# Optimization experiments

Hardware: AMD Instinct MI355X
Metric: run time of the kernel (lower is better)

The kernel has to match this reference:

```python
import jax, jax.numpy as jnp
import numpy as np

NUM_QUANTIZERS = 8
CODEBOOK_SIZE = 1024
DIM = 64
B, N = 8, 8192


def setup_inputs() -> dict:
    key = jax.random.key(0)
    kx, kc = jax.random.split(key)
    x = jax.random.normal(kx, (B, N, DIM), dtype=jnp.float32)
    # one codebook per quantizer stage (shared_codebook=False)
    codebooks = jax.random.normal(kc, (NUM_QUANTIZERS, CODEBOOK_SIZE, DIM), dtype=jnp.float32)
    return {"x": x, "codebooks": codebooks}


def reference(x, codebooks):
    """Residual VQ: sequential nearest-codebook lookup with residual subtraction.

    x:         [b, n, d]
    codebooks: [Q, K, d]
    returns quantized_out: [b, n, d]
    """

    def step(carry, cb):
        residual, qout = carry                       # [b,n,d], [b,n,d]
        # squared euclidean distances, [b,n,K]
        r_sq = jnp.sum(residual * residual, axis=-1, keepdims=True)
        c_sq = jnp.sum(cb * cb, axis=-1)             # [K]
        dots = jnp.einsum('bnd,kd->bnk', residual, cb)
        dist = r_sq - 2.0 * dots + c_sq              # [b,n,K]
        idx = jnp.argmin(dist, axis=-1)              # [b,n]
        quant = cb[idx]                              # [b,n,d] gather
        # straight-through estimator (VectorQuantize forward)
        quant_st = residual + jax.lax.stop_gradient(quant - residual)
        new_residual = residual - jax.lax.stop_gradient(quant)
        return (new_residual, qout + quant_st), idx

    init = (x, jnp.zeros_like(x))
    (residual, quantized_out), all_indices = jax.lax.scan(step, init, codebooks)
    return quantized_out
```

## Files before the change

kernel.cpp:

```cpp
#include <hip/hip_runtime.h>

#define NQ 8
#define KCODES 1024
#define D 64
#define CHUNK 64
#define TPB 256
#define TOKPB 64
#define BIAS 96.0f

using short8 = __attribute__((ext_vector_type(8))) short;
using f32x4  = __attribute__((ext_vector_type(4))) float;

static __device__ __forceinline__ unsigned bf16_rne_bits(float f) {
    unsigned u = __float_as_uint(f);
    return (u + 0x7fffu + ((u >> 16) & 1u)) >> 16;
}
static __device__ __forceinline__ unsigned umn(unsigned a, unsigned b) { return a < b ? a : b; }
static __device__ __forceinline__ unsigned umx(unsigned a, unsigned b) { return a > b ? a : b; }
static __device__ __forceinline__ unsigned umed3(unsigned a, unsigned b, unsigned c) {
    unsigned d;
    asm("v_med3_u32 %0, %1, %2, %3" : "=v"(d) : "v"(a), "v"(b), "v"(c));
    return d;
}

__global__ __launch_bounds__(256) void prep_cb(const float* __restrict__ cb,
                                               int4* __restrict__ ws_cb) {
    int id = blockIdx.x * 256 + threadIdx.x;
    int n_rel = id & 63;
    int plane = (id >> 6) & 15;
    int ch    = (id >> 10) & 15;
    int q     = id >> 14;
    int g = plane & 3, kt = (plane >> 2) & 1, term = plane >> 3;
    int n = ch * CHUNK + n_rel;
    const float* src = cb + ((size_t)(q * KCODES + n)) * D + kt * 32 + g * 8;
    union { short s[8]; int4 v; } u;
    #pragma unroll
    for (int j = 0; j < 8; ++j) {
        float f = -src[j];
        unsigned hb = bf16_rne_bits(f);
        if (term == 0) {
            u.s[j] = (short)hb;
        } else {
            float lo = f - __uint_as_float(hb << 16);
            u.s[j] = (short)bf16_rne_bits(lo);
        }
    }
    ws_cb[id] = u.v;
}

__global__ __launch_bounds__(256) void prep_csq(const float* __restrict__ cb,
                                                float* __restrict__ ws_csq,
                                                float* __restrict__ ws_csqh) {
    int id = blockIdx.x * 256 + threadIdx.x;
    const float* c = cb + (size_t)id * D;
    float s0 = 0.f, s1 = 0.f, s2 = 0.f, s3 = 0.f;
    #pragma unroll
    for (int j = 0; j < 16; ++j) {
        s0 = fmaf(c[4*j+0], c[4*j+0], s0);
        s1 = fmaf(c[4*j+1], c[4*j+1], s1);
        s2 = fmaf(c[4*j+2], c[4*j+2], s2);
        s3 = fmaf(c[4*j+3], c[4*j+3], s3);
    }
    float cs = (s0 + s1) + (s2 + s3);
    ws_csq[id]  = cs;
    ws_csqh[id] = 0.5f * cs + BIAS;
}

__global__ __launch_bounds__(TPB, 4) void rvq_mfma(
    const float* __restrict__ x,
    const float* __restrict__ cb,
    const int4* __restrict__ ws_cb,
    const float* __restrict__ ws_csq,
    float* __restrict__ out)
{
    __shared__ __align__(16) float lds_resid[TOKPB * 68];
    __shared__ __align__(16) float lds_csqh_q[KCODES];
    __shared__ unsigned lds_cand[2][TOKPB * 3];
    __shared__ int      lds_pick[TOKPB];

    const int tid   = threadIdx.x;
    const int lane  = tid & 63;
    const int wave  = tid >> 6;
    const int group = wave >> 1;
    const int half  = wave & 1;
    const int g     = lane >> 4;
    const int c     = lane & 15;
    const int tok0  = blockIdx.x * TOKPB;
    const float* ws_csqh = ws_csq + 8192;

    {
        const int t = tid >> 2, part = tid & 3;
        const float4* xp = (const float4*)(x + (size_t)(tok0 + t) * D + part * 16);
        float4* rr = (float4*)(lds_resid + t * 68 + part * 16);
        #pragma unroll
        for (int k2 = 0; k2 < 4; ++k2) rr[k2] = xp[k2];
    }

    const int lid = (g << 6) + (half << 4) + c;
    const int sdo = (half << 4) + c;

    for (int q = 0; q < NQ; ++q) {
        {
            const float4 v = *(const float4*)(ws_csqh + (q << 10) + (tid << 2));
            *(float4*)(lds_csqh_q + (tid << 2)) = v;
        }
        __syncthreads();

        short8 ah0[2], ah1[2], al0[2], al1[2];
        #pragma unroll
        for (int s = 0; s < 2; ++s) {
            const float* rr = lds_resid + (group * 32 + s * 16 + c) * 68;
            float4 f0 = *(const float4*)(rr + 8 * g);
            float4 f1 = *(const float4*)(rr + 8 * g + 4);
            float4 f2 = *(const float4*)(rr + 32 + 8 * g);
            float4 f3 = *(const float4*)(rr + 36 + 8 * g);
            const float* v0 = (const float*)&f0;
            const float* v1 = (const float*)&f1;
            const float* v2 = (const float*)&f2;
            const float* v3 = (const float*)&f3;
            #pragma unroll
            for (int j = 0; j < 4; ++j) {
                float a = v0[j], b = v1[j], e = v2[j], f = v3[j];
                unsigned ha = bf16_rne_bits(a);
                unsigned hb = bf16_rne_bits(b);
                unsigned he = bf16_rne_bits(e);
                unsigned hf = bf16_rne_bits(f);
                ah0[s][j]   = (short)ha;  ah0[s][4+j] = (short)hb;
                ah1[s][j]   = (short)he;  ah1[s][4+j] = (short)hf;
                al0[s][j]   = (short)bf16_rne_bits(a - __uint_as_float(ha << 16));
                al0[s][4+j] = (short)bf16_rne_bits(b - __uint_as_float(hb << 16));
                al1[s][j]   = (short)bf16_rne_bits(e - __uint_as_float(he << 16));
                al1[s][4+j] = (short)bf16_rne_bits(f - __uint_as_float(hf << 16));
            }
        }

        unsigned T1[2][4], T2[2][4], T3[2][4];
        #pragma unroll
        for (int s = 0; s < 2; ++s)
            #pragma unroll
            for (int r = 0; r < 4; ++r) { T1[s][r] = 0xFFFFFFFFu; T2[s][r] = 0xFFFFFFFFu; T3[s][r] = 0xFFFFFFFFu; }

        const int4* fpq = ws_cb + ((size_t)q << 14) + lid;
        short8 nb0 = *(const short8*)(fpq);
        short8 nb1 = *(const short8*)(fpq + 256);
        short8 nb2 = *(const short8*)(fpq + 512);
        short8 nb3 = *(const short8*)(fpq + 768);
        #pragma unroll 1
        for (int ch = 0; ch < 32; ++ch) {
            const short8 bh0 = nb0, bh1 = nb1, bl0 = nb2, bl1 = nb3;
            if (ch < 31) {
                const int chn = ch + 1;
                const int4* fpn = fpq + ((chn >> 1) << 10) + ((chn & 1) << 5);
                nb0 = *(const short8*)(fpn);
                nb1 = *(const short8*)(fpn + 256);
                nb2 = *(const short8*)(fpn + 512);
                nb3 = *(const short8*)(fpn + 768);
            }
            const int cv = (ch << 5) + sdo;
            const float sd = lds_csqh_q[cv];
            const unsigned codev = (unsigned)cv;
            #pragma unroll
            for (int s = 0; s < 2; ++s) {
                f32x4 acc = {sd, sd, sd, sd};
                acc = __builtin_amdgcn_mfma_f32_16x16x32_bf16(ah0[s], bh0, acc, 0, 0, 0);
                acc = __builtin_amdgcn_mfma_f32_16x16x32_bf16(ah1[s], bh1, acc, 0, 0, 0);
                acc = __builtin_amdgcn_mfma_f32_16x16x32_bf16(al0[s], bh0, acc, 0, 0, 0);
                acc = __builtin_amdgcn_mfma_f32_16x16x32_bf16(ah0[s], bl0, acc, 0, 0, 0);
                acc = __builtin_amdgcn_mfma_f32_16x16x32_bf16(al1[s], bh1, acc, 0, 0, 0);
                acc = __builtin_amdgcn_mfma_f32_16x16x32_bf16(ah1[s], bl1, acc, 0, 0, 0);
                #pragma unroll
                for (int r = 0; r < 4; ++r) {
                    const unsigned p = (__float_as_uint(acc[r]) & 0xFFFFFC00u) | codev;
                    const unsigned t1o = T1[s][r], t2o = T2[s][r];
                    T1[s][r] = umn(t1o, p);
                    T2[s][r] = umed3(t1o, t2o, p);
                    T3[s][r] = umed3(t2o, T3[s][r], p);
                }
            }
        }

        #pragma unroll
        for (int st = 1; st <= 8; st <<= 1) {
            #pragma unroll
            for (int s = 0; s < 2; ++s) {
                #pragma unroll
                for (int r = 0; r < 4; ++r) {
                    unsigned o1 = (unsigned)__shfl_xor((int)T1[s][r], st);
                    unsigned o2 = (unsigned)__shfl_xor((int)T2[s][r], st);
                    unsigned o3 = (unsigned)__shfl_xor((int)T3[s][r], st);
                    unsigned x1 = umn(T1[s][r], o1), y1 = umx(T1[s][r], o1);
                    unsigned x2 = umn(T2[s][r], o2), y2 = umx(T2[s][r], o2);
                    unsigned x3 = umn(T3[s][r], o3);
                    T1[s][r] = x1;
                    T3[s][r] = umed3(y1, x2, umn(y2, x3));
                    T2[s][r] = umn(y1, x2);
                }
            }
        }

        if (c == 0) {
            #pragma unroll
            for (int s = 0; s < 2; ++s)
                #pragma unroll
                for (int r = 0; r < 4; ++r) {
                    const int idx = (group * 32 + s * 16 + g * 4 + r) * 3;
                    lds_cand[half][idx + 0] = T1[s][r];
                    lds_cand[half][idx + 1] = T2[s][r];
                    lds_cand[half][idx + 2] = T3[s][r];
                }
        }
        __syncthreads();

        {
            const int t4  = lane >> 2;
            const int sel = lane & 3;
            const int row = group * 32 + half * 16 + t4;
            unsigned a1 = lds_cand[0][row * 3 + 0];
            unsigned a2 = lds_cand[0][row * 3 + 1];
            unsigned a3 = lds_cand[0][row * 3 + 2];
            unsigned b1 = lds_cand[1][row * 3 + 0];
            unsigned b2 = lds_cand[1][row * 3 + 1];
            unsigned b3 = lds_cand[1][row * 3 + 2];
            unsigned x1 = umn(a1, b1), y1 = umx(a1, b1);
            unsigned x2 = umn(a2, b2), y2 = umx(a2, b2);
            unsigned x3 = umn(a3, b3);
            unsigned m1 = x1;
            unsigned m2 = umn(y1, x2);
            unsigned m3 = umed3(y1, x2, umn(y2, x3));
            const unsigned psel = (sel == 0) ? m1 : ((sel == 1) ? m2 : m3);
            const int cd = (int)(psel & 1023u);

            const float4* rrv = (const float4*)(lds_resid + row * 68);
            const float4* cpv = (const float4*)(cb + ((size_t)(q * KCODES + cd)) * D);
            float ax = 0.f, ay = 0.f, az = 0.f, aw = 0.f;
            #pragma unroll
            for (int j = 0; j < 16; ++j) {
                float4 rv = rrv[j];
                float4 cv = cpv[j];
                ax = fmaf(rv.x, cv.x, ax);
                ay = fmaf(rv.y, cv.y, ay);
                az = fmaf(rv.z, cv.z, az);
                aw = fmaf(rv.w, cv.w, aw);
            }
            float dot = (ax + ay) + (az + aw);
            float dd = fmaf(dot, -2.0f, ws_csq[q * KCODES + cd]);

            const int base = lane & ~3;
            float d0 = __shfl(dd, base);
            float d1 = __shfl(dd, base + 1);
            float d2 = __shfl(dd, base + 2);
            int cc0 = (int)(m1 & 1023u);
            int cc1 = (int)(m2 & 1023u);
            int cc2 = (int)(m3 & 1023u);
            float db = d0; int pick = cc0;
            if (d1 < db || (d1 == db && cc1 < pick)) { db = d1; pick = cc1; }
            if (d2 < db || (d2 == db && cc2 < pick)) { db = d2; pick = cc2; }
            if (sel == 0) lds_pick[row] = pick;
        }
        __syncthreads();

        {
            const int t = tid >> 2, part = tid & 3;
            const int ifin = lds_pick[t];
            const float4* cp = (const float4*)(cb + ((size_t)(q * KCODES + ifin)) * D + part * 16);
            float4* rr = (float4*)(lds_resid + t * 68 + part * 16);
            #pragma unroll
            for (int k2 = 0; k2 < 4; ++k2) {
                float4 rv = rr[k2], cv = cp[k2];
                rv.x -= cv.x; rv.y -= cv.y; rv.z -= cv.z; rv.w -= cv.w;
                rr[k2] = rv;
            }
        }
    }

    __syncthreads();
    {
        const int t = tid >> 2, part = tid & 3;
        const float4* xp = (const float4*)(x + (size_t)(tok0 + t) * D + part * 16);
        const float4* rr = (const float4*)(lds_resid + t * 68 + part * 16);
        float4* op = (float4*)(out + (size_t)(tok0 + t) * D + part * 16);
        #pragma unroll
        for (int k2 = 0; k2 < 4; ++k2) {
            float4 xv = xp[k2], rv = rr[k2];
            float4 o;
            o.x = xv.x - rv.x; o.y = xv.y - rv.y;
            o.z = xv.z - rv.z; o.w = xv.w - rv.w;
            op[k2] = o;
        }
    }
}

extern "C" void kernel_launch(void* const* d_in, const int* in_sizes, int n_in,
                              void* d_out, int out_size, void* d_ws, size_t ws_size,
                              hipStream_t stream) {
    const float* x  = (const float*)d_in[0];
    const float* cb = (const float*)d_in[1];
    float* out = (float*)d_out;

    int4*  ws_cb   = (int4*)d_ws;
    float* ws_csq  = (float*)((char*)d_ws + (size_t)2 * 1024 * 1024);
    float* ws_csqh = ws_csq + 8192;

    prep_cb <<<512, 256, 0, stream>>>(cb, ws_cb);
    prep_csq<<< 32, 256, 0, stream>>>(cb, ws_csq, ws_csqh);

    const int n_tokens = in_sizes[0] / D;
    const int grid = n_tokens / TOKPB;
    rvq_mfma<<<grid, TPB, 0, stream>>>(x, cb, ws_cb, ws_csq, out);
}
```

Before: 346.0 us.

## Halve tokens per block and drop codebook prefetch to raise occupancy

Cuts tokens per block from 64 to 32, so each wave keeps one 16-token MFMA tile instead of two. Launch bounds are raised to allow 8 blocks per CU. The register double-buffered prefetch of the next codebook chunk is replaced by direct loads inside the loop. The aim is to free registers and hide latency through more resident waves, at the cost of loading each codebook fragment twice as often per token and of some duplicated candidate-merge work across waves.

```diff
diff --git a/kernel.cpp b/kernel.cpp
--- a/kernel.cpp
+++ b/kernel.cpp
@@ -5,7 +5,7 @@
 #define D 64
 #define CHUNK 64
 #define TPB 256
-#define TOKPB 64
+#define TOKPB 32
 #define BIAS 96.0f
 
 using short8 = __attribute__((ext_vector_type(8))) short;
@@ -66,7 +66,7 @@
     ws_csqh[id] = 0.5f * cs + BIAS;
 }
 
-__global__ __launch_bounds__(TPB, 4) void rvq_mfma(
+__global__ __launch_bounds__(TPB, 8) void rvq_mfma(
     const float* __restrict__ x,
     const float* __restrict__ cb,
     const int4* __restrict__ ws_cb,
@@ -89,11 +89,11 @@
     const float* ws_csqh = ws_csq + 8192;
 
     {
-        const int t = tid >> 2, part = tid & 3;
-        const float4* xp = (const float4*)(x + (size_t)(tok0 + t) * D + part * 16);
-        float4* rr = (float4*)(lds_resid + t * 68 + part * 16);
-        #pragma unroll
-        for (int k2 = 0; k2 < 4; ++k2) rr[k2] = xp[k2];
+        const int t = tid >> 3, part = tid & 7;
+        const float4* xp = (const float4*)(x + (size_t)(tok0 + t) * D + part * 8);
+        float4* rr = (float4*)(lds_resid + t * 68 + part * 8);
+        rr[0] = xp[0];
+        rr[1] = xp[1];
     }
 
     const int lid = (g << 6) + (half << 4) + c;
@@ -106,10 +106,9 @@
         }
         __syncthreads();
 
-        short8 ah0[2], ah1[2], al0[2], al1[2];
-        #pragma unroll
-        for (int s = 0; s < 2; ++s) {
-            const float* rr = lds_resid + (group * 32 + s * 16 + c) * 68;
+        short8 ah0, ah1, al0, al1;
+        {
+            const float* rr = lds_resid + (group * 16 + c) * 68;
             float4 f0 = *(const float4*)(rr + 8 * g);
             float4 f1 = *(const float4*)(rr + 8 * g + 4);
             float4 f2 = *(const float4*)(rr + 32 + 8 * g);
@@ -125,96 +124,78 @@
                 unsigned hb = bf16_rne_bits(b);
                 unsigned he = bf16_rne_bits(e);
                 unsigned hf = bf16_rne_bits(f);
-                ah0[s][j]   = (short)ha;  ah0[s][4+j] = (short)hb;
-                ah1[s][j]   = (short)he;  ah1[s][4+j] = (short)hf;
-                al0[s][j]   = (short)bf16_rne_bits(a - __uint_as_float(ha << 16));
-                al0[s][4+j] = (short)bf16_rne_bits(b - __uint_as_float(hb << 16));
-                al1[s][j]   = (short)bf16_rne_bits(e - __uint_as_float(he << 16));
-                al1[s][4+j] = (short)bf16_rne_bits(f - __uint_as_float(hf << 16));
-            }
-        }
-
-        unsigned T1[2][4], T2[2][4], T3[2][4];
+                ah0[j]   = (short)ha;  ah0[4+j] = (short)hb;
+                ah1[j]   = (short)he;  ah1[4+j] = (short)hf;
+                al0[j]   = (short)bf16_rne_bits(a - __uint_as_float(ha << 16));
+                al0[4+j] = (short)bf16_rne_bits(b - __uint_as_float(hb << 16));
+                al1[j]   = (short)bf16_rne_bits(e - __uint_as_float(he << 16));
+                al1[4+j] = (short)bf16_rne_bits(f - __uint_as_float(hf << 16));
+            }
+        }
+
+        unsigned T1[4], T2[4], T3[4];
         #pragma unroll
-        for (int s = 0; s < 2; ++s)
-            #pragma unroll
-            for (int r = 0; r < 4; ++r) { T1[s][r] = 0xFFFFFFFFu; T2[s][r] = 0xFFFFFFFFu; T3[s][r] = 0xFFFFFFFFu; }
+        for (int r = 0; r < 4; ++r) { T1[r] = 0xFFFFFFFFu; T2[r] = 0xFFFFFFFFu; T3[r] = 0xFFFFFFFFu; }
 
         const int4* fpq = ws_cb + ((size_t)q << 14) + lid;
-        short8 nb0 = *(const short8*)(fpq);
-        short8 nb1 = *(const short8*)(fpq + 256);
-        short8 nb2 = *(const short8*)(fpq + 512);
-        short8 nb3 = *(const short8*)(fpq + 768);
         #pragma unroll 1
         for (int ch = 0; ch < 32; ++ch) {
-            const short8 bh0 = nb0, bh1 = nb1, bl0 = nb2, bl1 = nb3;
-            if (ch < 31) {
-                const int chn = ch + 1;
-                const int4* fpn = fpq + ((chn >> 1) << 10) + ((chn & 1) << 5);
-                nb0 = *(const short8*)(fpn);
-                nb1 = *(const short8*)(fpn + 256);
-                nb2 = *(const short8*)(fpn + 512);
-                nb3 = *(const short8*)(fpn + 768);
-            }
+            const int4* fp = fpq + ((ch >> 1) << 10) + ((ch & 1) << 5);
+            const short8 bh0 = *(const short8*)(fp);
+            const short8 bh1 = *(const short8*)(fp + 256);
+            const short8 bl0 = *(const short8*)(fp + 512);
+            const short8 bl1 = *(const short8*)(fp + 768);
             const int cv = (ch << 5) + sdo;
             const float sd = lds_csqh_q[cv];
             const unsigned codev = (unsigned)cv;
-            #pragma unroll
-            for (int s = 0; s < 2; ++s) {
-                f32x4 acc = {sd, sd, sd, sd};
-                acc = __builtin_amdgcn_mfma_f32_16x16x32_bf16(ah0[s], bh0, acc, 0, 0, 0);
-                acc = __builtin_amdgcn_mfma_f32_16x16x32_bf16(ah1[s], bh1, acc, 0, 0, 0);
-                acc = __builtin_amdgcn_mfma_f32_16x16x32_bf16(al0[s], bh0, acc, 0, 0, 0);
-                acc = __builtin_amdgcn_mfma_f32_16x16x32_bf16(ah0[s], bl0, acc, 0, 0, 0);
-                acc = __builtin_amdgcn_mfma_f32_16x16x32_bf16(al1[s], bh1, acc, 0, 0, 0);
-                acc = __builtin_amdgcn_mfma_f32_16x16x32_bf16(ah1[s], bl1, acc, 0, 0, 0);
-                #pragma unroll
-                for (int r = 0; r < 4; ++r) {
-                    const unsigned p = (__float_as_uint(acc[r]) & 0xFFFFFC00u) | codev;
-                    const unsigned t1o = T1[s][r], t2o = T2[s][r];
-                    T1[s][r] = umn(t1o, p);
-                    T2[s][r] = umed3(t1o, t2o, p);
-                    T3[s][r] = umed3(t2o, T3[s][r], p);
-                }
+            f32x4 acc = {sd, sd, sd, sd};
+            acc = __builtin_amdgcn_mfma_f32_16x16x32_bf16(ah0, bh0, acc, 0, 0, 0);
+            acc = __builtin_amdgcn_mfma_f32_16x16x32_bf16(ah1, bh1, acc, 0, 0, 0);
+            acc = __builtin_amdgcn_mfma_f32_16x16x32_bf16(al0, bh0, acc, 0, 0, 0);
+            acc = __builtin_amdgcn_mfma_f32_16x16x32_bf16(ah0, bl0, acc, 0, 0, 0);
+            acc = __builtin_amdgcn_mfma_f32_16x16x32_bf16(al1, bh1, acc, 0, 0, 0);
+            acc = __builtin_amdgcn_mfma_f32_16x16x32_bf16(ah1, bl1, acc, 0, 0, 0);
+            #pragma unroll
+            for (int r = 0; r < 4; ++r) {
+                const unsigned p = (__float_as_uint(acc[r]) & 0xFFFFFC00u) | codev;
+                const unsigned t1o = T1[r], t2o = T2[r];
+                T1[r] = umn(t1o, p);
+                T2[r] = umed3(t1o, t2o, p);
+                T3[r] = umed3(t2o, T3[r], p);
             }
         }
 
         #pragma unroll
         for (int st = 1; st <= 8; st <<= 1) {
             #pragma unroll
-            for (int s = 0; s < 2; ++s) {
-                #pragma unroll
-                for (int r = 0; r < 4; ++r) {
-                    unsigned o1 = (unsigned)__shfl_xor((int)T1[s][r], st);
-                    unsigned o2 = (unsigned)__shfl_xor((int)T2[s][r], st);
-                    unsigned o3 = (unsigned)__shfl_xor((int)T3[s][r], st);
-                    unsigned x1 = umn(T1[s][r], o1), y1 = umx(T1[s][r], o1);
-                    unsigned x2 = umn(T2[s][r], o2), y2 = umx(T2[s][r], o2);
-                    unsigned x3 = umn(T3[s][r], o3);
-                    T1[s][r] = x1;
-                    T3[s][r] = umed3(y1, x2, umn(y2, x3));
-                    T2[s][r] = umn(y1, x2);
-                }
+            for (int r = 0; r < 4; ++r) {
+                unsigned o1 = (unsigned)__shfl_xor((int)T1[r], st);
+                unsigned o2 = (unsigned)__shfl_xor((int)T2[r], st);
+                unsigned o3 = (unsigned)__shfl_xor((int)T3[r], st);
+                unsigned x1 = umn(T1[r], o1), y1 = umx(T1[r], o1);
+                unsigned x2 = umn(T2[r], o2), y2 = umx(T2[r], o2);
+                unsigned x3 = umn(T3[r], o3);
+                T1[r] = x1;
+                T3[r] = umed3(y1, x2, umn(y2, x3));
+                T2[r] = umn(y1, x2);
             }
         }
 
         if (c == 0) {
             #pragma unroll
-            for (int s = 0; s < 2; ++s)
-                #pragma unroll
-                for (int r = 0; r < 4; ++r) {
-                    const int idx = (group * 32 + s * 16 + g * 4 + r) * 3;
-                    lds_cand[half][idx + 0] = T1[s][r];
-                    lds_cand[half][idx + 1] = T2[s][r];
-                    lds_cand[half][idx + 2] = T3[s][r];
-                }
+            for (int r = 0; r < 4; ++r) {
+                const int idx = (group * 16 + g * 4 + r) * 3;
+                lds_cand[half][idx + 0] = T1[r];
+                lds_cand[half][idx + 1] = T2[r];
+                lds_cand[half][idx + 2] = T3[r];
+            }
         }
         __syncthreads();
 
         {
             const int t4  = lane >> 2;
             const int sel = lane & 3;
-            const int row = group * 32 + half * 16 + t4;
+            const int row = half * 16 + t4;
             unsigned a1 = lds_cand[0][row * 3 + 0];
             unsigned a2 = lds_cand[0][row * 3 + 1];
             unsigned a3 = lds_cand[0][row * 3 + 2];
@@ -260,12 +241,12 @@
         __syncthreads();
 
         {
-            const int t = tid >> 2, part = tid & 3;
+            const int t = tid >> 3, part = tid & 7;
             const int ifin = lds_pick[t];
-            const float4* cp = (const float4*)(cb + ((size_t)(q * KCODES + ifin)) * D + part * 16);
-            float4* rr = (float4*)(lds_resid + t * 68 + part * 16);
-            #pragma unroll
-            for (int k2 = 0; k2 < 4; ++k2) {
+            const float4* cp = (const float4*)(cb + ((size_t)(q * KCODES + ifin)) * D + part * 8);
+            float4* rr = (float4*)(lds_resid + t * 68 + part * 8);
+            #pragma unroll
+            for (int k2 = 0; k2 < 2; ++k2) {
                 float4 rv = rr[k2], cv = cp[k2];
                 rv.x -= cv.x; rv.y -= cv.y; rv.z -= cv.z; rv.w -= cv.w;
                 rr[k2] = rv;
@@ -275,12 +256,12 @@
 
     __syncthreads();
     {
-        const int t = tid >> 2, part = tid & 3;
-        const float4* xp = (const float4*)(x + (size_t)(tok0 + t) * D + part * 16);
-        const float4* rr = (const float4*)(lds_resid + t * 68 + part * 16);
-        float4* op = (float4*)(out + (size_t)(tok0 + t) * D + part * 16);
+        const int t = tid >> 3, part = tid & 7;
+        const float4* xp = (const float4*)(x + (size_t)(tok0 + t) * D + part * 8);
+        const float4* rr = (const float4*)(lds_resid + t * 68 + part * 8);
+        float4* op = (float4*)(out + (size_t)(tok0 + t) * D + part * 8);
         #pragma unroll
-        for (int k2 = 0; k2 < 4; ++k2) {
+        for (int k2 = 0; k2 < 2; ++k2) {
             float4 xv = xp[k2], rv = rr[k2];
             float4 o;
             o.x = xv.x - rv.x; o.y = xv.y - rv.y;
```

Result: slower. 475.2 us (+37.3%).

## Triple-buffer codebook fragment prefetch and load csq directly from global

Applied to the files above, without the earlier changes.

Replaces the single-stage register prefetch of codebook fragments with a three-slot rotating pipeline, so loads are issued two chunks ahead of the MFMA work that uses them. The per-code half-norm bias is now read straight from global memory per chunk instead of being staged through shared memory, which removes one LDS buffer and its store. This hides more global-load latency at the cost of roughly 40 extra VGPRs, which could reduce occupancy under the 4-waves launch bound.

```diff
diff --git a/kernel.cpp b/kernel.cpp
--- a/kernel.cpp
+++ b/kernel.cpp
@@ -66,6 +66,38 @@
     ws_csqh[id] = 0.5f * cs + BIAS;
 }
 
+#define ISSUE(S, CH) do {                                                                 \
+    const int4* fp_ = fpq + (((CH) >> 1) << 10) + (((CH) & 1) << 5);                      \
+    S##f0 = *(const short8*)(fp_);                                                        \
+    S##f1 = *(const short8*)(fp_ + 256);                                                  \
+    S##f2 = *(const short8*)(fp_ + 512);                                                  \
+    S##f3 = *(const short8*)(fp_ + 768);                                                  \
+    S##sd = sdq[(CH) << 5];                                                               \
+} while (0)
+
+#define COMPUTE(S, CH) do {                                                               \
+    const unsigned codev_ = (unsigned)(((CH) << 5) + sdo);                                \
+    const float sd_ = S##sd;                                                              \
+    _Pragma("unroll")                                                                     \
+    for (int s = 0; s < 2; ++s) {                                                         \
+        f32x4 acc = {sd_, sd_, sd_, sd_};                                                 \
+        acc = __builtin_amdgcn_mfma_f32_16x16x32_bf16(ah0[s], S##f0, acc, 0, 0, 0);       \
+        acc = __builtin_amdgcn_mfma_f32_16x16x32_bf16(ah1[s], S##f1, acc, 0, 0, 0);       \
+        acc = __builtin_amdgcn_mfma_f32_16x16x32_bf16(al0[s], S##f0, acc, 0, 0, 0);       \
+        acc = __builtin_amdgcn_mfma_f32_16x16x32_bf16(ah0[s], S##f2, acc, 0, 0, 0);       \
+        acc = __builtin_amdgcn_mfma_f32_16x16x32_bf16(al1[s], S##f1, acc, 0, 0, 0);       \
+        acc = __builtin_amdgcn_mfma_f32_16x16x32_bf16(ah1[s], S##f3, acc, 0, 0, 0);       \
+        _Pragma("unroll")                                                                 \
+        for (int r = 0; r < 4; ++r) {                                                     \
+            const unsigned p = (__float_as_uint(acc[r]) & 0xFFFFFC00u) | codev_;          \
+            const unsigned t1o = T1[s][r], t2o = T2[s][r];                                \
+            T1[s][r] = umn(t1o, p);                \
+            T2[s][r] = umed3(t1o, t2o, p);         \
+            T3[s][r] = umed3(t2o, T3[s][r], p);    \
+        }                                                                                 \
+    }                                                                                     \
+} while (0)
+
 __global__ __launch_bounds__(TPB, 4) void rvq_mfma(
     const float* __restrict__ x,
     const float* __restrict__ cb,
@@ -74,7 +106,6 @@
     float* __restrict__ out)
 {
     __shared__ __align__(16) float lds_resid[TOKPB * 68];
-    __shared__ __align__(16) float lds_csqh_q[KCODES];
     __shared__ unsigned lds_cand[2][TOKPB * 3];
     __shared__ int      lds_pick[TOKPB];
 
@@ -99,12 +130,18 @@
     const int lid = (g << 6) + (half << 4) + c;
     const int sdo = (half << 4) + c;
 
+    short8 P0f0, P0f1, P0f2, P0f3;  float P0sd;
+    short8 P1f0, P1f1, P1f2, P1f3;  float P1sd;
+    short8 P2f0, P2f1, P2f2, P2f3;  float P2sd;
+
     for (int q = 0; q < NQ; ++q) {
-        {
-            const float4 v = *(const float4*)(ws_csqh + (q << 10) + (tid << 2));
-            *(float4*)(lds_csqh_q + (tid << 2)) = v;
-        }
         __syncthreads();
+
+        const int4*  fpq = ws_cb + ((size_t)q << 14) + lid;
+        const float* sdq = ws_csqh + (q << 10) + sdo;
+
+        ISSUE(P0, 0);
+        ISSUE(P1, 1);
 
         short8 ah0[2], ah1[2], al0[2], al1[2];
         #pragma unroll
@@ -140,44 +177,15 @@
             #pragma unroll
             for (int r = 0; r < 4; ++r) { T1[s][r] = 0xFFFFFFFFu; T2[s][r] = 0xFFFFFFFFu; T3[s][r] = 0xFFFFFFFFu; }
 
-        const int4* fpq = ws_cb + ((size_t)q << 14) + lid;
-        short8 nb0 = *(const short8*)(fpq);
-        short8 nb1 = *(const short8*)(fpq + 256);
-        short8 nb2 = *(const short8*)(fpq + 512);
-        short8 nb3 = *(const short8*)(fpq + 768);
         #pragma unroll 1
-        for (int ch = 0; ch < 32; ++ch) {
-            const short8 bh0 = nb0, bh1 = nb1, bl0 = nb2, bl1 = nb3;
-            if (ch < 31) {
-                const int chn = ch + 1;
-                const int4* fpn = fpq + ((chn >> 1) << 10) + ((chn & 1) << 5);
-                nb0 = *(const short8*)(fpn);
-                nb1 = *(const short8*)(fpn + 256);
-                nb2 = *(const short8*)(fpn + 512);
-                nb3 = *(const short8*)(fpn + 768);
-            }
-            const int cv = (ch << 5) + sdo;
-            const float sd = lds_csqh_q[cv];
-            const unsigned codev = (unsigned)cv;
-            #pragma unroll
-            for (int s = 0; s < 2; ++s) {
-                f32x4 acc = {sd, sd, sd, sd};
-                acc = __builtin_amdgcn_mfma_f32_16x16x32_bf16(ah0[s], bh0, acc, 0, 0, 0);
-                acc = __builtin_amdgcn_mfma_f32_16x16x32_bf16(ah1[s], bh1, acc, 0, 0, 0);
-                acc = __builtin_amdgcn_mfma_f32_16x16x32_bf16(al0[s], bh0, acc, 0, 0, 0);
-                acc = __builtin_amdgcn_mfma_f32_16x16x32_bf16(ah0[s], bl0, acc, 0, 0, 0);
-                acc = __builtin_amdgcn_mfma_f32_16x16x32_bf16(al1[s], bh1, acc, 0, 0, 0);
-                acc = __builtin_amdgcn_mfma_f32_16x16x32_bf16(ah1[s], bl1, acc, 0, 0, 0);
-                #pragma unroll
-                for (int r = 0; r < 4; ++r) {
-                    const unsigned p = (__float_as_uint(acc[r]) & 0xFFFFFC00u) | codev;
-                    const unsigned t1o = T1[s][r], t2o = T2[s][r];
-                    T1[s][r] = umn(t1o, p);
-                    T2[s][r] = umed3(t1o, t2o, p);
-                    T3[s][r] = umed3(t2o, T3[s][r], p);
-                }
-            }
-        }
+        for (int cp = 0; cp < 10; ++cp) {
+            const int ch = cp * 3;
+            ISSUE(P2, ch + 2); COMPUTE(P0, ch);
+            ISSUE(P0, ch + 3); COMPUTE(P1, ch + 1);
+            ISSUE(P1, ch + 4); COMPUTE(P2, ch + 2);
+        }
+        COMPUTE(P0, 30);
+        COMPUTE(P1, 31);
 
         #pragma unroll
         for (int st = 1; st <= 8; st <<= 1) {
```

New measurement: 339.0 us (median of 2 runs). -2.0%, faster.
